# Optimization experiments

Hardware: AMD Instinct MI355X
Metric: run time of the kernel (lower is better)

Reference implementation:

```python
import jax, jax.numpy as jnp
import numpy as np

N_HEADS = 16
WINDOW = 256


def setup_inputs() -> dict:
    key = jax.random.key(0)
    ks = jax.random.split(key, 6)
    B, S, D = 2, 2048, 1024
    std = 0.02
    x = jax.random.normal(ks[0], (B, S, D), dtype=jnp.float32)
    wq = jax.random.normal(ks[1], (D, D), dtype=jnp.float32) * std
    wk = jax.random.normal(ks[2], (D, D), dtype=jnp.float32) * std
    wv = jax.random.normal(ks[3], (D, D), dtype=jnp.float32) * std
    wo = jax.random.normal(ks[4], (D, D), dtype=jnp.float32) * std
    bq = jnp.zeros((D,), jnp.float32)
    bk = jnp.zeros((D,), jnp.float32)
    bv = jnp.zeros((D,), jnp.float32)
    bo = jnp.zeros((D,), jnp.float32)
    return {"x": x, "wq": wq, "bq": bq, "wk": wk, "bk": bk,
            "wv": wv, "bv": bv, "wo": wo, "bo": bo}


def _sliding_window_bias(seq_len: int) -> jnp.ndarray:
    # allowed iff |i - j| <= WINDOW  ->  0.0, else -inf  (matches torch loop mask)
    i = jnp.arange(seq_len)[:, None]
    j = jnp.arange(seq_len)[None, :]
    allowed = jnp.abs(i - j) <= WINDOW
    return jnp.where(allowed, 0.0, -jnp.inf).astype(jnp.float32)


def reference(x, wq, bq, wk, bk, wv, bv, wo, bo):
    B, S, D = x.shape
    H = N_HEADS
    dh = D // H
    scale = dh ** -0.5
    # nn.Linear: y = x @ W^T + b
    q = (x @ wq.T + bq).reshape(B, S, H, dh).transpose(0, 2, 1, 3)  # [B,H,S,dh]
    k = (x @ wk.T + bk).reshape(B, S, H, dh).transpose(0, 2, 1, 3)
    v = (x @ wv.T + bv).reshape(B, S, H, dh).transpose(0, 2, 1, 3)
    scores = jnp.einsum('bhqd,bhkd->bhqk', q, k) * scale  # [B,H,S,S]
    scores = scores + _sliding_window_bias(S)[None, None]
    attn = jax.nn.softmax(scores, axis=-1)
    out = jnp.einsum('bhqk,bhkd->bhqd', attn, v)  # [B,H,S,dh]
    out = out.transpose(0, 2, 1, 3).reshape(B, S, D)
    return out @ wo.T + bo
```

## Files before the change

### kernel.cpp

```cpp
#include <hip/hip_runtime.h>
#include <stdint.h>

static constexpr int Ss = 2048;
static constexpr int Dd = 1024;
static constexpr int Hh = 16;
static constexpr int DH = 64;

typedef short bf16x8 __attribute__((ext_vector_type(8)));
typedef float f32x4 __attribute__((ext_vector_type(4)));
typedef uint32_t u32x4 __attribute__((ext_vector_type(4)));

#define LOG2E 1.4426950408889634f

__device__ __forceinline__ uint16_t f2bf(float f) {
  uint32_t u = __builtin_bit_cast(uint32_t, f);
  u += 0x7fffu + ((u >> 16) & 1u);
  return (uint16_t)(u >> 16);
}
__device__ __forceinline__ float bf2f(uint16_t h) {
  uint32_t u = ((uint32_t)h) << 16;
  return __builtin_bit_cast(float, u);
}
__device__ __forceinline__ uint32_t cvtpk(float a, float b) {
  uint32_t r;
  asm("v_cvt_pk_bf16_f32 %0, %1, %2" : "=v"(r) : "v"(a), "v"(b));
  return r;
}

template <int CTRL>
__device__ __forceinline__ float dppf(float x) {
  return __builtin_bit_cast(float,
      __builtin_amdgcn_update_dpp(0, __builtin_bit_cast(int, x), CTRL, 0xF, 0xF, true));
}
__device__ __forceinline__ float rowsum16(float v) {
  v += dppf<0x128>(v);
  v += dppf<0x124>(v);
  v += dppf<0x122>(v);
  v += dppf<0x121>(v);
  return v;
}
__device__ __forceinline__ float fexp2(float x) { return __builtin_amdgcn_exp2f(x); }

#define GAS(p) ((const __attribute__((address_space(1))) uint32_t*)(p))
#define LAS(p) ((__attribute__((address_space(3))) uint32_t*)(p))

__global__ void cvt_w(const float* __restrict__ w0, const float* __restrict__ w1,
                      const float* __restrict__ w2, const float* __restrict__ w3,
                      uint16_t* __restrict__ o0, uint16_t* __restrict__ o1,
                      uint16_t* __restrict__ o2, uint16_t* __restrict__ o3) {
  int bid = blockIdx.x;
  int t = bid >> 10;
  const float* in = (t == 0) ? w0 : (t == 1) ? w1 : (t == 2) ? w2 : w3;
  uint16_t* out = (t == 0) ? o0 : (t == 1) ? o1 : (t == 2) ? o2 : o3;
  int i = (bid & 1023) * 256 + threadIdx.x;
  float4 v = reinterpret_cast<const float4*>(in)[i];
  ushort4 o;
  o.x = f2bf(v.x); o.y = f2bf(v.y); o.z = f2bf(v.z); o.w = f2bf(v.w);
  reinterpret_cast<ushort4*>(out)[i] = o;
}

__global__ __launch_bounds__(256, 2) void gemm_qkv(
    const float* __restrict__ X,
    const uint16_t* __restrict__ W0, const uint16_t* __restrict__ W1, const uint16_t* __restrict__ W2,
    const float* __restrict__ b0, const float* __restrict__ b1, const float* __restrict__ b2,
    uint16_t* __restrict__ O0, uint16_t* __restrict__ O1, uint16_t* __restrict__ O2) {
  constexpr int K = 1024;
  __shared__ __align__(16) uint8_t ldsA[2][128 * 128];
  __shared__ __align__(16) uint8_t ldsB[128 * 128];

  const int tid = threadIdx.x, w = tid >> 6, lane = tid & 63;
  const int q = lane & 15, g = lane >> 4;
  const int wm = w >> 1, wn = w & 1;
  const int bx = blockIdx.x, by = blockIdx.y, z = blockIdx.z;
  const uint16_t* Wp = (z == 0) ? W0 : (z == 1) ? W1 : W2;
  const float* bp = (z == 0) ? b0 : (z == 1) ? b1 : b2;
  uint16_t* Op = (z == 0) ? O0 : (z == 1) ? O1 : O2;

  int arow[4], aelem[4];
#pragma unroll
  for (int i = 0; i < 4; ++i) {
    int Lb = w * 4096 + i * 1024 + lane * 16;
    int row = Lb >> 7, cb = Lb & 127;
    arow[i] = row;
    aelem[i] = (cb ^ ((row & 7) << 4)) >> 1;
  }

  f32x4 acc[4][4] = {};
  float4 ar[4][2];

#pragma unroll
  for (int i = 0; i < 4; ++i) {
    const float* s = X + (size_t)(bx * 128 + arow[i]) * K + aelem[i];
    ar[i][0] = *(const float4*)s;
    ar[i][1] = *(const float4*)(s + 4);
  }

  const int nkt = K >> 6;
  for (int kt = 0; kt < nkt; ++kt) {
    const int k0 = kt << 6;
    const int cur = kt & 1;

    __builtin_amdgcn_s_barrier();
    __builtin_amdgcn_sched_barrier(0);
#pragma unroll
    for (int i = 0; i < 4; ++i) {
      int Lb = w * 4096 + i * 1024 + lane * 16;
      int row = Lb >> 7, cb = Lb & 127;
      const uint16_t* srcB = Wp + (size_t)(by * 128 + row) * K + k0 + ((cb ^ ((row & 7) << 4)) >> 1);
      __builtin_amdgcn_global_load_lds(GAS(srcB), LAS(ldsB + w * 4096 + i * 1024), 16, 0, 0);
    }
    __builtin_amdgcn_sched_barrier(0);
#pragma unroll
    for (int i = 0; i < 4; ++i) {
      u32x4 pk;
      pk[0] = cvtpk(ar[i][0].x, ar[i][0].y);
      pk[1] = cvtpk(ar[i][0].z, ar[i][0].w);
      pk[2] = cvtpk(ar[i][1].x, ar[i][1].y);
      pk[3] = cvtpk(ar[i][1].z, ar[i][1].w);
      *(u32x4*)(ldsA[cur] + w * 4096 + i * 1024 + lane * 16) = pk;
    }
    __builtin_amdgcn_sched_barrier(0);
    if (kt + 1 < nkt) {
#pragma unroll
      for (int i = 0; i < 4; ++i) {
        const float* s = X + (size_t)(bx * 128 + arow[i]) * K + (k0 + 64) + aelem[i];
        ar[i][0] = *(const float4*)s;
        ar[i][1] = *(const float4*)(s + 4);
      }
      __builtin_amdgcn_sched_barrier(0);
      asm volatile("s_waitcnt vmcnt(8) lgkmcnt(0)" ::: "memory");
    } else {
      asm volatile("s_waitcnt vmcnt(0) lgkmcnt(0)" ::: "memory");
    }
    __builtin_amdgcn_sched_barrier(0);
    __builtin_amdgcn_s_barrier();
    __builtin_amdgcn_sched_barrier(0);

    bf16x8 af[4][2], bfg[4][2];
#pragma unroll
    for (int mi = 0; mi < 4; ++mi)
#pragma unroll
      for (int s = 0; s < 2; ++s) {
        int row = wm * 64 + mi * 16 + q;
        int cb = (16 * g + 64 * s) ^ ((row & 7) << 4);
        af[mi][s] = *(const bf16x8*)(ldsA[cur] + row * 128 + cb);
      }
#pragma unroll
    for (int ni = 0; ni < 4; ++ni)
#pragma unroll
      for (int s = 0; s < 2; ++s) {
        int row = wn * 64 + ni * 16 + q;
        int cb = (16 * g + 64 * s) ^ ((row & 7) << 4);
        bfg[ni][s] = *(const bf16x8*)(ldsB + row * 128 + cb);
      }
#pragma unroll
    for (int mi = 0; mi < 4; ++mi)
#pragma unroll
      for (int ni = 0; ni < 4; ++ni) {
        acc[mi][ni] = __builtin_amdgcn_mfma_f32_16x16x32_bf16(af[mi][0], bfg[ni][0], acc[mi][ni], 0, 0, 0);
        acc[mi][ni] = __builtin_amdgcn_mfma_f32_16x16x32_bf16(af[mi][1], bfg[ni][1], acc[mi][ni], 0, 0, 0);
      }
  }

  float bias[4];
#pragma unroll
  for (int ni = 0; ni < 4; ++ni) bias[ni] = bp[by * 128 + wn * 64 + ni * 16 + q];
#pragma unroll
  for (int mi = 0; mi < 4; ++mi)
#pragma unroll
    for (int ni = 0; ni < 4; ++ni)
#pragma unroll
      for (int r = 0; r < 4; ++r) {
        int m = bx * 128 + wm * 64 + mi * 16 + 4 * g + r;
        int n = by * 128 + wn * 64 + ni * 16 + q;
        float v = acc[mi][ni][r] + bias[ni];
        int b = m >> 11, s = m & 2047, h = n >> 6, d = n & 63;
        Op[(((size_t)(b * Hh + h) * Ss + s) << 6) + d] = f2bf(v);
      }
}

__global__ __launch_bounds__(256, 2) void gemm_out(
    const uint16_t* __restrict__ A, const uint16_t* __restrict__ W,
    const float* __restrict__ bp, float* __restrict__ O, int M, int N, int K) {
  __shared__ __align__(16) uint8_t ldsA[128 * 128];
  __shared__ __align__(16) uint8_t ldsB[64 * 128];

  const int tid = threadIdx.x, w = tid >> 6, lane = tid & 63;
  const int q = lane & 15, g = lane >> 4;
  const int wm = w >> 1, wn = w & 1;
  const int bx = blockIdx.x, by = blockIdx.y;

  f32x4 acc[4][2] = {};

  const int nkt = K >> 6;
  for (int kt = 0; kt < nkt; ++kt) {
    const int k0 = kt << 6;
    __syncthreads();
#pragma unroll
    for (int i = 0; i < 4; ++i) {
      int Lb = w * 4096 + i * 1024 + lane * 16;
      int row = Lb >> 7, cb = Lb & 127;
      const uint16_t* srcA = A + (size_t)(bx * 128 + row) * K + k0 + ((cb ^ ((row & 7) << 4)) >> 1);
      __builtin_amdgcn_global_load_lds(GAS(srcA), LAS(ldsA + w * 4096 + i * 1024), 16, 0, 0);
    }
#pragma unroll
    for (int i = 0; i < 2; ++i) {
      int Lb = w * 2048 + i * 1024 + lane * 16;
      int row = Lb >> 7, cb = Lb & 127;
      const uint16_t* srcB = W + (size_t)(by * 64 + row) * K + k0 + ((cb ^ ((row & 7) << 4)) >> 1);
      __builtin_amdgcn_global_load_lds(GAS(srcB), LAS(ldsB + w * 2048 + i * 1024), 16, 0, 0);
    }
    __syncthreads();

    bf16x8 af[4][2], bfg[2][2];
#pragma unroll
    for (int mi = 0; mi < 4; ++mi)
#pragma unroll
      for (int s = 0; s < 2; ++s) {
        int row = wm * 64 + mi * 16 + q;
        int cb = (16 * g + 64 * s) ^ ((row & 7) << 4);
        af[mi][s] = *(const bf16x8*)(ldsA + row * 128 + cb);
      }
#pragma unroll
    for (int ni = 0; ni < 2; ++ni)
#pragma unroll
      for (int s = 0; s < 2; ++s) {
        int row = wn * 32 + ni * 16 + q;
        int cb = (16 * g + 64 * s) ^ ((row & 7) << 4);
        bfg[ni][s] = *(const bf16x8*)(ldsB + row * 128 + cb);
      }
#pragma unroll
    for (int mi = 0; mi < 4; ++mi)
#pragma unroll
      for (int ni = 0; ni < 2; ++ni) {
        acc[mi][ni] = __builtin_amdgcn_mfma_f32_16x16x32_bf16(af[mi][0], bfg[ni][0], acc[mi][ni], 0, 0, 0);
        acc[mi][ni] = __builtin_amdgcn_mfma_f32_16x16x32_bf16(af[mi][1], bfg[ni][1], acc[mi][ni], 0, 0, 0);
      }
  }

  float bias[2];
#pragma unroll
  for (int ni = 0; ni < 2; ++ni) bias[ni] = bp[by * 64 + wn * 32 + ni * 16 + q];
#pragma unroll
  for (int mi = 0; mi < 4; ++mi)
#pragma unroll
    for (int ni = 0; ni < 2; ++ni)
#pragma unroll
      for (int r = 0; r < 4; ++r) {
        int m = bx * 128 + wm * 64 + mi * 16 + 4 * g + r;
        int n = by * 64 + wn * 32 + ni * 16 + q;
        O[(size_t)m * N + n] = acc[mi][ni][r] + bias[ni];
      }
}

__global__ __launch_bounds__(512, 4) void attn_swa(
    const uint16_t* __restrict__ Qg, const uint16_t* __restrict__ Kg,
    const uint16_t* __restrict__ Vg, uint16_t* __restrict__ Og) {
  __shared__ __align__(16) uint8_t ldsK[2][64 * 128];
  __shared__ __align__(16) uint8_t ldsVt[2][64 * 128];
  __shared__ __align__(16) uint8_t ldsP[8][2048];

  const int tid = threadIdx.x, w = tid >> 6, lane = tid & 63;
  const int q = lane & 15, g = lane >> 4;
  const int qb = blockIdx.x, bh = blockIdx.y;
  const size_t hbase = (size_t)bh * Ss * DH;
  const uint16_t* Qp = Qg + hbase;
  const uint16_t* Kp = Kg + hbase;
  const uint16_t* Vp = Vg + hbase;
  const int q0 = qb * 128;
  const int qw = q0 + w * 16;

  bf16x8 aq[2];
#pragma unroll
  for (int s = 0; s < 2; ++s) {
    bf16x8 t = *(const bf16x8*)(Qp + (size_t)(qw + q) * DH + s * 32 + g * 8);
#pragma unroll
    for (int j = 0; j < 8; ++j) {
      float f = bf2f((uint16_t)t[j]) * 0.125f;
      t[j] = (short)f2bf(f);
    }
    aq[s] = t;
  }

  f32x4 accO[4] = {};
  float lrun[4] = {0.f, 0.f, 0.f, 0.f};

  const int t0 = (q0 >= 256) ? (q0 - 256) : 0;
  const int t1 = (q0 + 384 <= Ss) ? (q0 + 384) : Ss;
  const int nt = (t1 - t0) >> 6;

  {
    int Lb = w * 1024 + lane * 16;
    int row = Lb >> 7, cb = Lb & 127;
    const uint16_t* srcK = Kp + (size_t)(t0 + row) * DH + ((cb ^ ((row & 7) << 4)) >> 1);
    __builtin_amdgcn_global_load_lds(GAS(srcK), LAS(ldsK[0] + w * 1024), 16, 0, 0);
  }
  bf16x8 v0 = *(const bf16x8*)(Vp + (size_t)(t0 + lane) * DH + w * 8);

  for (int t = 0; t < nt; ++t) {
    const int kb0 = t0 + (t << 6);
    const int cur = t & 1, nxt = cur ^ 1;

    asm volatile("s_waitcnt vmcnt(0)" ::: "memory");
    uint8_t* Vt = ldsVt[cur];
#pragma unroll
    for (int j = 0; j < 8; ++j) {
      int c = w * 8 + j;
      *(uint16_t*)(Vt + c * 128 + ((2 * lane) ^ (j << 4))) = (uint16_t)v0[j];
    }
    asm volatile("s_waitcnt lgkmcnt(0)" ::: "memory");
    __builtin_amdgcn_sched_barrier(0);
    __builtin_amdgcn_s_barrier();
    __builtin_amdgcn_sched_barrier(0);

    if (t + 1 < nt) {
      int Lb = w * 1024 + lane * 16;
      int row = Lb >> 7, cb = Lb & 127;
      const uint16_t* srcK = Kp + (size_t)(kb0 + 64 + row) * DH + ((cb ^ ((row & 7) << 4)) >> 1);
      __builtin_amdgcn_global_load_lds(GAS(srcK), LAS(ldsK[nxt] + w * 1024), 16, 0, 0);
      v0 = *(const bf16x8*)(Vp + (size_t)(kb0 + 64 + lane) * DH + w * 8);
    }

    const int dtile = kb0 - qw;
    if (dtile >= -319 && dtile <= 271) {
      const uint8_t* Kl = ldsK[cur];
      f32x4 sacc[4] = {};
#pragma unroll
      for (int kb = 0; kb < 4; ++kb) {
        int row = kb * 16 + q;
#pragma unroll
        for (int s = 0; s < 2; ++s) {
          int cb = (16 * g + 64 * s) ^ ((row & 7) << 4);
          bf16x8 bk = *(const bf16x8*)(Kl + row * 128 + cb);
          sacc[kb] = __builtin_amdgcn_mfma_f32_16x16x32_bf16(aq[s], bk, sacc[kb], 0, 0, 0);
        }
      }
      if (dtile < -192 || dtile > 192) {
#pragma unroll
        for (int kb = 0; kb < 4; ++kb) {
          int key = kb0 + kb * 16 + q;
#pragma unroll
          for (int r = 0; r < 4; ++r) {
            int qi = qw + 4 * g + r;
            int dd = qi - key;
            bool ok = (dd <= 256) && (dd >= -256);
            sacc[kb][r] = ok ? sacc[kb][r] : -1e30f;
          }
        }
      }
      uint8_t* Pl = ldsP[w];
#pragma unroll
      for (int r = 0; r < 4; ++r) {
        float p0 = fexp2(sacc[0][r] * LOG2E);
        float p1 = fexp2(sacc[1][r] * LOG2E);
        float p2 = fexp2(sacc[2][r] * LOG2E);
        float p3 = fexp2(sacc[3][r] * LOG2E);
        float rs = rowsum16((p0 + p1) + (p2 + p3));
        lrun[r] += rs;
        int prow = 4 * g + r;
        int sw = (prow & 7) << 4;
        uint8_t* Pr = Pl + prow * 128;
        uint32_t pk01 = cvtpk(p0, p1), pk23 = cvtpk(p2, p3);
        *(uint16_t*)(Pr + ((2 * q) ^ sw))      = (uint16_t)pk01;
        *(uint16_t*)(Pr + ((2 * q + 32) ^ sw)) = (uint16_t)(pk01 >> 16);
        *(uint16_t*)(Pr + ((2 * q + 64) ^ sw)) = (uint16_t)pk23;
        *(uint16_t*)(Pr + ((2 * q + 96) ^ sw)) = (uint16_t)(pk23 >> 16);
      }
      bf16x8 ap[2];
#pragma unroll
      for (int s = 0; s < 2; ++s) {
        int cb = (16 * g + 64 * s) ^ ((q & 7) << 4);
        ap[s] = *(const bf16x8*)(Pl + q * 128 + cb);
      }
#pragma unroll
      for (int db = 0; db < 4; ++db) {
        int vr = db * 16 + q;
#pragma unroll
        for (int s = 0; s < 2; ++s) {
          int cb = (64 * s + 16 * g) ^ ((vr & 7) << 4);
          bf16x8 bvf = *(const bf16x8*)(ldsVt[cur] + vr * 128 + cb);
          accO[db] = __builtin_amdgcn_mfma_f32_16x16x32_bf16(ap[s], bvf, accO[db], 0, 0, 0);
        }
      }
    }
  }

  const int b2 = bh >> 4, h = bh & 15;
#pragma unroll
  for (int r = 0; r < 4; ++r) {
    float inv = 1.0f / lrun[r];
    int qi = qw + 4 * g + r;
    size_t rowbase = ((size_t)(b2 * Ss + qi)) * Dd + h * DH;
#pragma unroll
    for (int db = 0; db < 4; ++db) {
      Og[rowbase + db * 16 + q] = f2bf(accO[db][r] * inv);
    }
  }
}

extern "C" void kernel_launch(void* const* d_in, const int* in_sizes, int n_in,
                              void* d_out, int out_size, void* d_ws, size_t ws_size,
                              hipStream_t stream) {
  const float* x  = (const float*)d_in[0];
  const float* wq = (const float*)d_in[1];
  const float* bq = (const float*)d_in[2];
  const float* wk = (const float*)d_in[3];
  const float* bk = (const float*)d_in[4];
  const float* wv = (const float*)d_in[5];
  const float* bv = (const float*)d_in[6];
  const float* wo = (const float*)d_in[7];
  const float* bo = (const float*)d_in[8];
  float* out = (float*)d_out;

  uint8_t* ws = (uint8_t*)d_ws;
  uint16_t* wqb = (uint16_t*)(ws + (size_t)(0u  << 20));
  uint16_t* wkb = (uint16_t*)(ws + (size_t)(2u  << 20));
  uint16_t* wvb = (uint16_t*)(ws + (size_t)(4u  << 20));
  uint16_t* wob = (uint16_t*)(ws + (size_t)(6u  << 20));
  uint16_t* Qb  = (uint16_t*)(ws + (size_t)(8u  << 20));
  uint16_t* Kb  = (uint16_t*)(ws + (size_t)(16u << 20));
  uint16_t* Vb  = (uint16_t*)(ws + (size_t)(24u << 20));
  uint16_t* AOb = (uint16_t*)(ws + (size_t)(32u << 20));

  cvt_w<<<4096, 256, 0, stream>>>(wq, wk, wv, wo, wqb, wkb, wvb, wob);

  gemm_qkv<<<dim3(32, 8, 3), 256, 0, stream>>>(
      x, wqb, wkb, wvb, bq, bk, bv, Qb, Kb, Vb);

  attn_swa<<<dim3(16, 32), 512, 0, stream>>>(Qb, Kb, Vb, AOb);

  gemm_out<<<dim3(32, 16), 256, 0, stream>>>(
      AOb, wob, bo, out, 4096, 1024, 1024);
}
```

Measured before the change: 81.57 us.

## Pre-convert X to bf16, double-buffer out-projection GEMM, raise MFMA priority

X is now converted to bf16 in the same pass as the weights, so the QKV GEMM loads both operands straight into LDS with global_load_lds instead of loading fp32 into registers and packing it. In exchange, the QKV GEMM loses its register-prefetch overlap and goes back to a single buffer with two barriers per step. The output GEMM gains LDS double buffering so the next tile's loads are issued before the current tile's MFMAs. The attention kernel wraps its MFMA blocks in s_setprio to favour matrix issue across waves. The extra conversion pass writes and rereads an 8 MB bf16 copy of X.

Result: faster. 78.94 us (-3.2%).

```diff
diff --git a/kernel.cpp b/kernel.cpp
--- a/kernel.cpp
+++ b/kernel.cpp
@@ -8,7 +8,6 @@
 
 typedef short bf16x8 __attribute__((ext_vector_type(8)));
 typedef float f32x4 __attribute__((ext_vector_type(4)));
-typedef uint32_t u32x4 __attribute__((ext_vector_type(4)));
 
 #define LOG2E 1.4426950408889634f
 
@@ -44,15 +43,25 @@
 #define GAS(p) ((const __attribute__((address_space(1))) uint32_t*)(p))
 #define LAS(p) ((__attribute__((address_space(3))) uint32_t*)(p))
 
-__global__ void cvt_w(const float* __restrict__ w0, const float* __restrict__ w1,
-                      const float* __restrict__ w2, const float* __restrict__ w3,
-                      uint16_t* __restrict__ o0, uint16_t* __restrict__ o1,
-                      uint16_t* __restrict__ o2, uint16_t* __restrict__ o3) {
+__global__ void cvt_all(const float* __restrict__ x,
+                        const float* __restrict__ w0, const float* __restrict__ w1,
+                        const float* __restrict__ w2, const float* __restrict__ w3,
+                        uint16_t* __restrict__ xb,
+                        uint16_t* __restrict__ o0, uint16_t* __restrict__ o1,
+                        uint16_t* __restrict__ o2, uint16_t* __restrict__ o3) {
   int bid = blockIdx.x;
-  int t = bid >> 10;
-  const float* in = (t == 0) ? w0 : (t == 1) ? w1 : (t == 2) ? w2 : w3;
-  uint16_t* out = (t == 0) ? o0 : (t == 1) ? o1 : (t == 2) ? o2 : o3;
-  int i = (bid & 1023) * 256 + threadIdx.x;
+  const float* in;
+  uint16_t* out;
+  int i;
+  if (bid < 4096) {
+    in = x; out = xb; i = bid * 256 + threadIdx.x;
+  } else {
+    int b2 = bid - 4096;
+    int t = b2 >> 10;
+    in = (t == 0) ? w0 : (t == 1) ? w1 : (t == 2) ? w2 : w3;
+    out = (t == 0) ? o0 : (t == 1) ? o1 : (t == 2) ? o2 : o3;
+    i = (b2 & 1023) * 256 + threadIdx.x;
+  }
   float4 v = reinterpret_cast<const float4*>(in)[i];
   ushort4 o;
   o.x = f2bf(v.x); o.y = f2bf(v.y); o.z = f2bf(v.z); o.w = f2bf(v.w);
@@ -60,12 +69,12 @@
 }
 
 __global__ __launch_bounds__(256, 2) void gemm_qkv(
-    const float* __restrict__ X,
+    const uint16_t* __restrict__ A,
     const uint16_t* __restrict__ W0, const uint16_t* __restrict__ W1, const uint16_t* __restrict__ W2,
     const float* __restrict__ b0, const float* __restrict__ b1, const float* __restrict__ b2,
     uint16_t* __restrict__ O0, uint16_t* __restrict__ O1, uint16_t* __restrict__ O2) {
   constexpr int K = 1024;
-  __shared__ __align__(16) uint8_t ldsA[2][128 * 128];
+  __shared__ __align__(16) uint8_t ldsA[128 * 128];
   __shared__ __align__(16) uint8_t ldsB[128 * 128];
 
   const int tid = threadIdx.x, w = tid >> 6, lane = tid & 63;
@@ -76,65 +85,23 @@
   const float* bp = (z == 0) ? b0 : (z == 1) ? b1 : b2;
   uint16_t* Op = (z == 0) ? O0 : (z == 1) ? O1 : O2;
 
-  int arow[4], aelem[4];
-#pragma unroll
-  for (int i = 0; i < 4; ++i) {
-    int Lb = w * 4096 + i * 1024 + lane * 16;
-    int row = Lb >> 7, cb = Lb & 127;
-    arow[i] = row;
-    aelem[i] = (cb ^ ((row & 7) << 4)) >> 1;
-  }
-
   f32x4 acc[4][4] = {};
-  float4 ar[4][2];
-
-#pragma unroll
-  for (int i = 0; i < 4; ++i) {
-    const float* s = X + (size_t)(bx * 128 + arow[i]) * K + aelem[i];
-    ar[i][0] = *(const float4*)s;
-    ar[i][1] = *(const float4*)(s + 4);
-  }
 
   const int nkt = K >> 6;
   for (int kt = 0; kt < nkt; ++kt) {
     const int k0 = kt << 6;
-    const int cur = kt & 1;
-
-    __builtin_amdgcn_s_barrier();
-    __builtin_amdgcn_sched_barrier(0);
+    __syncthreads();
 #pragma unroll
     for (int i = 0; i < 4; ++i) {
       int Lb = w * 4096 + i * 1024 + lane * 16;
       int row = Lb >> 7, cb = Lb & 127;
-      const uint16_t* srcB = Wp + (size_t)(by * 128 + row) * K + k0 + ((cb ^ ((row & 7) << 4)) >> 1);
+      int col = (cb ^ ((row & 7) << 4)) >> 1;
+      const uint16_t* srcA = A + (size_t)(bx * 128 + row) * K + k0 + col;
+      __builtin_amdgcn_global_load_lds(GAS(srcA), LAS(ldsA + w * 4096 + i * 1024), 16, 0, 0);
+      const uint16_t* srcB = Wp + (size_t)(by * 128 + row) * K + k0 + col;
       __builtin_amdgcn_global_load_lds(GAS(srcB), LAS(ldsB + w * 4096 + i * 1024), 16, 0, 0);
     }
-    __builtin_amdgcn_sched_barrier(0);
-#pragma unroll
-    for (int i = 0; i < 4; ++i) {
-      u32x4 pk;
-      pk[0] = cvtpk(ar[i][0].x, ar[i][0].y);
-      pk[1] = cvtpk(ar[i][0].z, ar[i][0].w);
-      pk[2] = cvtpk(ar[i][1].x, ar[i][1].y);
-      pk[3] = cvtpk(ar[i][1].z, ar[i][1].w);
-      *(u32x4*)(ldsA[cur] + w * 4096 + i * 1024 + lane * 16) = pk;
-    }
-    __builtin_amdgcn_sched_barrier(0);
-    if (kt + 1 < nkt) {
-#pragma unroll
-      for (int i = 0; i < 4; ++i) {
-        const float* s = X + (size_t)(bx * 128 + arow[i]) * K + (k0 + 64) + aelem[i];
-        ar[i][0] = *(const float4*)s;
-        ar[i][1] = *(const float4*)(s + 4);
-      }
-      __builtin_amdgcn_sched_barrier(0);
-      asm volatile("s_waitcnt vmcnt(8) lgkmcnt(0)" ::: "memory");
-    } else {
-      asm volatile("s_waitcnt vmcnt(0) lgkmcnt(0)" ::: "memory");
-    }
-    __builtin_amdgcn_sched_barrier(0);
-    __builtin_amdgcn_s_barrier();
-    __builtin_amdgcn_sched_barrier(0);
+    __syncthreads();
 
     bf16x8 af[4][2], bfg[4][2];
 #pragma unroll
@@ -143,7 +110,7 @@
       for (int s = 0; s < 2; ++s) {
         int row = wm * 64 + mi * 16 + q;
         int cb = (16 * g + 64 * s) ^ ((row & 7) << 4);
-        af[mi][s] = *(const bf16x8*)(ldsA[cur] + row * 128 + cb);
+        af[mi][s] = *(const bf16x8*)(ldsA + row * 128 + cb);
       }
 #pragma unroll
     for (int ni = 0; ni < 4; ++ni)
@@ -182,8 +149,8 @@
 __global__ __launch_bounds__(256, 2) void gemm_out(
     const uint16_t* __restrict__ A, const uint16_t* __restrict__ W,
     const float* __restrict__ bp, float* __restrict__ O, int M, int N, int K) {
-  __shared__ __align__(16) uint8_t ldsA[128 * 128];
-  __shared__ __align__(16) uint8_t ldsB[64 * 128];
+  __shared__ __align__(16) uint8_t ldsA[2][128 * 128];
+  __shared__ __align__(16) uint8_t ldsB[2][64 * 128];
 
   const int tid = threadIdx.x, w = tid >> 6, lane = tid & 63;
   const int q = lane & 15, g = lane >> 4;
@@ -192,25 +159,35 @@
 
   f32x4 acc[4][2] = {};
 
+  const int Lb4 = lane * 16;
+  auto stage = [&](int kt, int buf) {
+    const int k0 = kt << 6;
+#pragma unroll
+    for (int i = 0; i < 4; ++i) {
+      int Lb = w * 4096 + i * 1024 + Lb4;
+      int row = Lb >> 7, cb = Lb & 127;
+      const uint16_t* srcA = A + (size_t)(bx * 128 + row) * K + k0 + ((cb ^ ((row & 7) << 4)) >> 1);
+      __builtin_amdgcn_global_load_lds(GAS(srcA), LAS(ldsA[buf] + w * 4096 + i * 1024), 16, 0, 0);
+    }
+#pragma unroll
+    for (int i = 0; i < 2; ++i) {
+      int Lb = w * 2048 + i * 1024 + Lb4;
+      int row = Lb >> 7, cb = Lb & 127;
+      const uint16_t* srcB = W + (size_t)(by * 64 + row) * K + k0 + ((cb ^ ((row & 7) << 4)) >> 1);
+      __builtin_amdgcn_global_load_lds(GAS(srcB), LAS(ldsB[buf] + w * 2048 + i * 1024), 16, 0, 0);
+    }
+  };
+
+  stage(0, 0);
+
   const int nkt = K >> 6;
   for (int kt = 0; kt < nkt; ++kt) {
-    const int k0 = kt << 6;
-    __syncthreads();
-#pragma unroll
-    for (int i = 0; i < 4; ++i) {
-      int Lb = w * 4096 + i * 1024 + lane * 16;
-      int row = Lb >> 7, cb = Lb & 127;
-      const uint16_t* srcA = A + (size_t)(bx * 128 + row) * K + k0 + ((cb ^ ((row & 7) << 4)) >> 1);
-      __builtin_amdgcn_global_load_lds(GAS(srcA), LAS(ldsA + w * 4096 + i * 1024), 16, 0, 0);
-    }
-#pragma unroll
-    for (int i = 0; i < 2; ++i) {
-      int Lb = w * 2048 + i * 1024 + lane * 16;
-      int row = Lb >> 7, cb = Lb & 127;
-      const uint16_t* srcB = W + (size_t)(by * 64 + row) * K + k0 + ((cb ^ ((row & 7) << 4)) >> 1);
-      __builtin_amdgcn_global_load_lds(GAS(srcB), LAS(ldsB + w * 2048 + i * 1024), 16, 0, 0);
-    }
-    __syncthreads();
+    const int cur = kt & 1;
+    asm volatile("s_waitcnt vmcnt(0)" ::: "memory");
+    __builtin_amdgcn_sched_barrier(0);
+    __builtin_amdgcn_s_barrier();
+    __builtin_amdgcn_sched_barrier(0);
+    if (kt + 1 < nkt) stage(kt + 1, cur ^ 1);
 
     bf16x8 af[4][2], bfg[2][2];
 #pragma unroll
@@ -219,7 +196,7 @@
       for (int s = 0; s < 2; ++s) {
         int row = wm * 64 + mi * 16 + q;
         int cb = (16 * g + 64 * s) ^ ((row & 7) << 4);
-        af[mi][s] = *(const bf16x8*)(ldsA + row * 128 + cb);
+        af[mi][s] = *(const bf16x8*)(ldsA[cur] + row * 128 + cb);
       }
 #pragma unroll
     for (int ni = 0; ni < 2; ++ni)
@@ -227,7 +204,7 @@
       for (int s = 0; s < 2; ++s) {
         int row = wn * 32 + ni * 16 + q;
         int cb = (16 * g + 64 * s) ^ ((row & 7) << 4);
-        bfg[ni][s] = *(const bf16x8*)(ldsB + row * 128 + cb);
+        bfg[ni][s] = *(const bf16x8*)(ldsB[cur] + row * 128 + cb);
       }
 #pragma unroll
     for (int mi = 0; mi < 4; ++mi)
@@ -325,6 +302,7 @@
     if (dtile >= -319 && dtile <= 271) {
       const uint8_t* Kl = ldsK[cur];
       f32x4 sacc[4] = {};
+      __builtin_amdgcn_s_setprio(1);
 #pragma unroll
       for (int kb = 0; kb < 4; ++kb) {
         int row = kb * 16 + q;
@@ -335,6 +313,7 @@
           sacc[kb] = __builtin_amdgcn_mfma_f32_16x16x32_bf16(aq[s], bk, sacc[kb], 0, 0, 0);
         }
       }
+      __builtin_amdgcn_s_setprio(0);
       if (dtile < -192 || dtile > 192) {
 #pragma unroll
         for (int kb = 0; kb < 4; ++kb) {
@@ -372,6 +351,7 @@
         int cb = (16 * g + 64 * s) ^ ((q & 7) << 4);
         ap[s] = *(const bf16x8*)(Pl + q * 128 + cb);
       }
+      __builtin_amdgcn_s_setprio(1);
 #pragma unroll
       for (int db = 0; db < 4; ++db) {
         int vr = db * 16 + q;
@@ -382,6 +362,7 @@
           accO[db] = __builtin_amdgcn_mfma_f32_16x16x32_bf16(ap[s], bvf, accO[db], 0, 0, 0);
         }
       }
+      __builtin_amdgcn_s_setprio(0);
     }
   }
 
@@ -413,19 +394,20 @@
   float* out = (float*)d_out;
 
   uint8_t* ws = (uint8_t*)d_ws;
-  uint16_t* wqb = (uint16_t*)(ws + (size_t)(0u  << 20));
-  uint16_t* wkb = (uint16_t*)(ws + (size_t)(2u  << 20));
-  uint16_t* wvb = (uint16_t*)(ws + (size_t)(4u  << 20));
-  uint16_t* wob = (uint16_t*)(ws + (size_t)(6u  << 20));
-  uint16_t* Qb  = (uint16_t*)(ws + (size_t)(8u  << 20));
-  uint16_t* Kb  = (uint16_t*)(ws + (size_t)(16u << 20));
-  uint16_t* Vb  = (uint16_t*)(ws + (size_t)(24u << 20));
-  uint16_t* AOb = (uint16_t*)(ws + (size_t)(32u << 20));
-
-  cvt_w<<<4096, 256, 0, stream>>>(wq, wk, wv, wo, wqb, wkb, wvb, wob);
+  uint16_t* xb  = (uint16_t*)(ws + (size_t)(0u  << 20));
+  uint16_t* wqb = (uint16_t*)(ws + (size_t)(8u  << 20));
+  uint16_t* wkb = (uint16_t*)(ws + (size_t)(10u << 20));
+  uint16_t* wvb = (uint16_t*)(ws + (size_t)(12u << 20));
+  uint16_t* wob = (uint16_t*)(ws + (size_t)(14u << 20));
+  uint16_t* Qb  = (uint16_t*)(ws + (size_t)(16u << 20));
+  uint16_t* Kb  = (uint16_t*)(ws + (size_t)(24u << 20));
+  uint16_t* Vb  = (uint16_t*)(ws + (size_t)(32u << 20));
+  uint16_t* AOb = (uint16_t*)(ws + (size_t)(40u << 20));
+
+  cvt_all<<<8192, 256, 0, stream>>>(x, wq, wk, wv, wo, xb, wqb, wkb, wvb, wob);
 
   gemm_qkv<<<dim3(32, 8, 3), 256, 0, stream>>>(
-      x, wqb, wkb, wvb, bq, bk, bv, Qb, Kb, Vb);
+      xb, wqb, wkb, wvb, bq, bk, bv, Qb, Kb, Vb);
 
   attn_swa<<<dim3(16, 32), 512, 0, stream>>>(Qb, Kb, Vb, AOb);
 
```
